# Optimization experiments

Hardware: AMD Instinct MI355X
Metric: run time of the kernel (lower is better)

## Reference

```python
import jax, jax.numpy as jnp
import numpy as np

N = 10000   # nodes
E = 100000  # edges
B = 64      # graphs
HID = 128


def setup_inputs() -> dict:
    key = jax.random.key(0)
    ks = iter(jax.random.split(key, 64))
    def nrm(shape, s=0.1):
        return jax.random.normal(next(ks), shape, dtype=jnp.float32) * s
    inp = {}
    inp["x"] = nrm((N, 1), 1.0)
    inp["node_type"] = jax.random.randint(next(ks), (N,), 0, 2)
    inp["edge_index"] = jax.random.randint(next(ks), (2, E), 0, N)
    inp["edge_attr"] = nrm((E, 1), 1.0)
    inp["batch"] = jnp.sort(jax.random.randint(next(ks), (N,), 0, B))
    inp["vp_w"] = nrm((1, HID)); inp["vp_b"] = nrm((HID,))
    inp["type_emb"] = nrm((2, HID))
    def conv(pre, fin, h, c):
        inp[pre + "_wl"] = nrm((fin, h * c)); inp[pre + "_bl"] = nrm((h * c,))
        inp[pre + "_wr"] = nrm((fin, h * c)); inp[pre + "_br"] = nrm((h * c,))
        inp[pre + "_we"] = nrm((1, h * c));  inp[pre + "_att"] = nrm((h, c))
        inp[pre + "_bias"] = nrm((h * c if pre != "c3" else c,))
    conv("c1", HID, 8, HID)
    conv("c2", HID * 8, 2, HID)
    conv("c3", HID * 2, 1, HID)
    inp["m1_w"] = nrm((HID, HID)); inp["m1_b"] = nrm((HID,))
    inp["ln1_g"] = jnp.ones((HID,), jnp.float32); inp["ln1_b"] = jnp.zeros((HID,), jnp.float32)
    inp["m2_w"] = nrm((HID, HID // 2)); inp["m2_b"] = nrm((HID // 2,))
    inp["ln2_g"] = jnp.ones((HID // 2,), jnp.float32); inp["ln2_b"] = jnp.zeros((HID // 2,), jnp.float32)
    inp["m3_w"] = nrm((HID // 2, 1)); inp["m3_b"] = nrm((1,))
    return inp


def _gatv2(x, src, dst, ea, wl, bl, wr, br, we, att, bias, heads, out_ch, concat):
    """PyG GATv2Conv (eval mode): add self-loops (edge_attr fill='mean' over dst),
    attn = (att * leaky_relu(Wl x_src + Wr x_dst + We e)).sum(-1), segment-softmax
    over destination, scatter-add of alpha * Wl x_src."""
    n = x.shape[0]
    ones = jnp.ones((ea.shape[0], 1), ea.dtype)
    deg = jax.ops.segment_sum(ones, dst, num_segments=n)
    loop_attr = jax.ops.segment_sum(ea, dst, num_segments=n) / jnp.maximum(deg, 1.0)
    ar = jnp.arange(n, dtype=src.dtype)
    src2 = jnp.concatenate([src, ar])
    dst2 = jnp.concatenate([dst, ar])
    ea2 = jnp.concatenate([ea, loop_attr], axis=0)
    xl = (x @ wl + bl).reshape(n, heads, out_ch)   # source transform
    xr = (x @ wr + br).reshape(n, heads, out_ch)   # target transform
    e = (ea2 @ we).reshape(-1, heads, out_ch)      # [E2, H, C]
    msg = xl[src2]                                 # [E2, H, C]
    z = jax.nn.leaky_relu(msg + xr[dst2] + e, 0.2)
    score = jnp.einsum('ehc,hc->eh', z, att)       # [E2, H]
    smax = jax.ops.segment_max(score, dst2, num_segments=n)
    ex = jnp.exp(score - smax[dst2])
    denom = jax.ops.segment_sum(ex, dst2, num_segments=n)
    alpha = ex / denom[dst2]
    out = jax.ops.segment_sum(alpha[:, :, None] * msg, dst2, num_segments=n)
    out = out.reshape(n, heads * out_ch) if concat else out.mean(axis=1)
    return out + bias


def _layernorm(v, g, b):
    mu = v.mean(-1, keepdims=True)
    var = v.var(-1, keepdims=True)
    return (v - mu) / jnp.sqrt(var + 1e-5) * g + b


def reference(x, node_type, edge_index, edge_attr, batch,
              vp_w, vp_b, type_emb,
              c1_wl, c1_bl, c1_wr, c1_br, c1_we, c1_att, c1_bias,
              c2_wl, c2_bl, c2_wr, c2_br, c2_we, c2_att, c2_bias,
              c3_wl, c3_bl, c3_wr, c3_br, c3_we, c3_att, c3_bias,
              m1_w, m1_b, ln1_g, ln1_b, m2_w, m2_b, ln2_g, ln2_b, m3_w, m3_b):
    src, dst = edge_index[0], edge_index[1]
    h = x @ vp_w + vp_b + type_emb[node_type]
    h = jax.nn.leaky_relu(_gatv2(h, src, dst, edge_attr, c1_wl, c1_bl, c1_wr, c1_br, c1_we, c1_att, c1_bias, 8, HID, True), 0.2)
    h = jax.nn.leaky_relu(_gatv2(h, src, dst, edge_attr, c2_wl, c2_bl, c2_wr, c2_br, c2_we, c2_att, c2_bias, 2, HID, True), 0.2)
    h = jax.nn.leaky_relu(_gatv2(h, src, dst, edge_attr, c3_wl, c3_bl, c3_wr, c3_br, c3_we, c3_att, c3_bias, 1, HID, False), 0.2)
    # masked global mean pool over node_type == 0
    w = (node_type == 0).astype(h.dtype)
    sums = jax.ops.segment_sum(h * w[:, None], batch, num_segments=B)
    cnts = jax.ops.segment_sum(w, batch, num_segments=B)
    pooled = sums / jnp.maximum(cnts, 1.0)[:, None]
    h1 = jax.nn.leaky_relu(_layernorm(pooled @ m1_w + m1_b, ln1_g, ln1_b), 0.2)
    h2 = jax.nn.leaky_relu(_layernorm(h1 @ m2_w + m2_b, ln2_g, ln2_b), 0.2)
    return (h2 @ m3_w + m3_b).squeeze(-1)
```

## Files before the change

### kernel.cpp

```cpp
#include <hip/hip_runtime.h>
#include <math.h>

#define NN 10000
#define NE 100000
#define E2 (NE + NN)
#define NBATCH 64

typedef short bf16x8 __attribute__((ext_vector_type(8)));
typedef float f32x4 __attribute__((ext_vector_type(4)));

__device__ __forceinline__ float lrelu(float v){ return fmaxf(v, 0.2f*v); }

__device__ __forceinline__ unsigned short f2bf(float x){
  unsigned int u = __float_as_uint(x);
  u += 0x7fffu + ((u >> 16) & 1u);
  return (unsigned short)(u >> 16);
}
__device__ __forceinline__ float bf2f(unsigned short u){
  return __uint_as_float(((unsigned int)u) << 16);
}

__global__ __launch_bounds__(256) void prep_kernel(
    const float* __restrict__ vp_w, const float* __restrict__ vp_b,
    const float* __restrict__ type_emb,
    const float* __restrict__ c1_wl, const float* __restrict__ c1_bl,
    const float* __restrict__ c1_wr, const float* __restrict__ c1_br,
    float* __restrict__ Ul, float* __restrict__ CTl,
    float* __restrict__ Ur, float* __restrict__ CTr,
    const float* __restrict__ c2_wl, const float* __restrict__ c2_wr,
    const float* __restrict__ c3_wl, const float* __restrict__ c3_wr,
    unsigned short* __restrict__ W2lT, unsigned short* __restrict__ W2rT,
    unsigned short* __restrict__ W3lT, unsigned short* __restrict__ W3rT,
    float* __restrict__ zbase, int zero_words)
{
  __shared__ float t[64][65];
  int b = blockIdx.x;
  int tid = threadIdx.x;
  if (b < 144){
    const float* in; unsigned short* out; int K, N, idx;
    if (b < 64)      { in=c2_wl; out=W2lT; K=1024; N=256; idx=b; }
    else if (b <128) { in=c2_wr; out=W2rT; K=1024; N=256; idx=b-64; }
    else if (b <136) { in=c3_wl; out=W3lT; K=256;  N=128; idx=b-128; }
    else             { in=c3_wr; out=W3rT; K=256;  N=128; idx=b-136; }
    int K64 = K >> 6;
    int kx = idx % K64, nx = idx / K64;
    int k0 = kx*64, n0 = nx*64;
    int lr = tid >> 4;
    int lc = (tid & 15) * 4;
#pragma unroll
    for (int i=0;i<4;++i){
      int r = lr + i*16;
      float4 v = *(const float4*)(in + (size_t)(k0+r)*N + n0 + lc);
      t[r][lc+0]=v.x; t[r][lc+1]=v.y; t[r][lc+2]=v.z; t[r][lc+3]=v.w;
    }
    __syncthreads();
    int sr = tid >> 3;
    int sc = (tid & 7) * 8;
#pragma unroll
    for (int i=0;i<2;++i){
      int n = sr + i*32;
      unsigned short tmp[8];
#pragma unroll
      for (int j=0;j<8;++j) tmp[j] = f2bf(t[sc+j][n]);
      unsigned short* op = out + (size_t)(n0+n)*K + k0 + sc;
      *(ushort4*)op       = make_ushort4(tmp[0],tmp[1],tmp[2],tmp[3]);
      *(ushort4*)(op + 4) = make_ushort4(tmp[4],tmp[5],tmp[6],tmp[7]);
    }
  } else if (b < 148){
    int j = (b-144)*256 + tid;
    float ul=0.f, c0l=0.f, c1l=0.f, ur=0.f, c0r=0.f, c1r=0.f;
    for (int k=0; k<128; ++k){
      float a = c1_wl[k*1024 + j], bb = c1_wr[k*1024 + j];
      float vw = vp_w[k], vb = vp_b[k], t0 = type_emb[k], t1 = type_emb[128+k];
      ul += vw*a; ur += vw*bb;
      c0l += (vb+t0)*a; c1l += (vb+t1)*a;
      c0r += (vb+t0)*bb; c1r += (vb+t1)*bb;
    }
    float bl = c1_bl[j], br = c1_br[j];
    Ul[j]=ul; Ur[j]=ur;
    CTl[j]      = c0l + bl;
    CTl[1024+j] = c1l + bl;
    CTr[j]      = c0r + br;
    CTr[1024+j] = c1r + br;
  } else {
    for (int i = (b-148)*256 + tid; i < zero_words; i += 32*256)
      zbase[i] = 0.f;
  }
}

__global__ void count_kernel(const int* __restrict__ dst, const float* __restrict__ ea,
                             int* __restrict__ deg, float* __restrict__ loop_sum){
  int e = blockIdx.x*256 + threadIdx.x;
  if (e < NE){
    int d = dst[e];
    atomicAdd(&deg[d], 1);
    atomicAdd(&loop_sum[d], ea[e]);
  }
}

__global__ __launch_bounds__(1024) void scan_kernel(const int* __restrict__ deg,
    const float* __restrict__ loop_sum, const float* __restrict__ x,
    const int* __restrict__ ntype,
    int* __restrict__ rowptr, int2* __restrict__ se, float2* __restrict__ xt){
  __shared__ int wtot[16];
  int tid = threadIdx.x;
  int lane = tid & 63, wid = tid >> 6;
  int base = tid*10;
  int d[10]; int run = 0;
#pragma unroll
  for (int j=0;j<10;++j){
    int i = base + j;
    int v = (i < NN) ? deg[i] : 0;
    run += v; d[j] = run;
  }
  int T = run;
  int incl = T;
#pragma unroll
  for (int off=1; off<64; off<<=1){
    int s = __shfl_up(incl, off, 64);
    if (lane >= off) incl += s;
  }
  if (lane == 63) wtot[wid] = incl;
  __syncthreads();
  int wpre = 0;
  for (int w2=0; w2<wid; ++w2) wpre += wtot[w2];
  int ebase = wpre + incl - T;
#pragma unroll
  for (int j=0;j<10;++j){
    int i = base + j;
    if (i < NN){
      int v = d[j] - ((j==0) ? 0 : d[j-1]);
      int rp2 = ebase + d[j] - v + i;
      rowptr[i] = rp2;
      float la = loop_sum[i] / fmaxf((float)v, 1.f);
      se[rp2] = make_int2(i, __float_as_int(la));
      xt[i] = make_float2(x[i], (float)ntype[i]);
    }
  }
  if (tid == 1023){
    int tot = wpre + incl + NN;
    rowptr[NN] = tot;
#pragma unroll
    for (int k=0; k<8; ++k) se[tot+k] = make_int2(0, 0);
  }
}

__global__ void fill_kernel(const int* __restrict__ src, const int* __restrict__ dst,
                            const float* __restrict__ ea, const int* __restrict__ rowptr,
                            int* __restrict__ rowctr, int2* __restrict__ se){
  int e = blockIdx.x*256 + threadIdx.x;
  if (e < NE){
    int d = dst[e];
    int p = rowptr[d] + 1 + atomicAdd(&rowctr[d], 1);
    se[p] = make_int2(src[e], __float_as_int(ea[e]));
  }
}

__global__ __launch_bounds__(256) void conv1_fused(
    const int* __restrict__ rowptr, const int2* __restrict__ se,
    const float2* __restrict__ xt,
    const float* __restrict__ Ul, const float* __restrict__ Ur,
    const float* __restrict__ CTl, const float* __restrict__ CTr,
    const float* __restrict__ we, const float* __restrict__ att,
    const float* __restrict__ bias, unsigned short* __restrict__ out)
{
  int n = blockIdx.x*2 + (threadIdx.x >> 7);
  if (n >= NN) return;
  int te = threadIdx.x & 127;
  int ch0 = te * 8;
  float ul[8], wev[8], a1[8], a2[8], cn0[8], cnd[8];
#pragma unroll
  for (int v=0; v<8; ++v){
    ul[v]=Ul[ch0+v]; wev[v]=we[ch0+v];
    float av = att[ch0+v]; a1[v]=0.6f*av; a2[v]=0.4f*av;
  }
  int beg = rowptr[n], cnt = rowptr[n+1]-beg;
  float2 xtn = xt[n];
  const float* ctr = (xtn.y != 0.f) ? (CTr+1024) : CTr;
#pragma unroll
  for (int v=0; v<8; ++v){
    float c0 = CTl[ch0+v], c1 = CTl[1024+ch0+v];
    cn0[v] = fmaf(xtn.x, Ur[ch0+v], ctr[ch0+v]) + c0;
    cnd[v] = c1 - c0;
  }
  const int2* sp = se + beg;
  int2 q0 = sp[0], q1 = sp[1], q2 = sp[2], q3 = sp[3];
  float2 x0 = xt[q0.x], x1 = xt[q1.x];
  float la_=0.f, lb_=0.f, s1a=0.f, s1b=0.f, sta=0.f, stb=0.f;
  int npair = cnt >> 1;
  for (int p=0; p<npair; ++p){
    int i = p*2;
    float2 x2 = xt[q2.x], x3 = xt[q3.x];
    int2 q4 = sp[i+4], q5 = sp[i+5];
    float xs0=x0.x, tf0=x0.y, ea0=__int_as_float(q0.y);
    float xs1=x1.x, tf1=x1.y, ea1=__int_as_float(q1.y);
    float p0a=0.f,p0b=0.f,p1a=0.f,p1b=0.f;
#pragma unroll
    for (int v=0; v<8; ++v){
      float z0 = fmaf(xs0, ul[v], fmaf(ea0, wev[v], fmaf(tf0, cnd[v], cn0[v])));
      float z1 = fmaf(xs1, ul[v], fmaf(ea1, wev[v], fmaf(tf1, cnd[v], cn0[v])));
      p0a = fmaf(a1[v], z0, p0a); p0b = fmaf(a2[v], fabsf(z0), p0b);
      p1a = fmaf(a1[v], z1, p1a); p1b = fmaf(a2[v], fabsf(z1), p1b);
    }
    float p0 = p0a+p0b, p1 = p1a+p1b;
#pragma unroll
    for (int mm=1; mm<16; mm<<=1){
      p0 += __shfl_xor(p0, mm, 16);
      p1 += __shfl_xor(p1, mm, 16);
    }
    float pe0 = __expf(p0), pe1 = __expf(p1);
    la_ += pe0; lb_ += pe1;
    s1a = fmaf(pe0, xs0, s1a); s1b = fmaf(pe1, xs1, s1b);
    sta = fmaf(pe0, tf0, sta); stb = fmaf(pe1, tf1, stb);
    q0=q2; x0=x2; q1=q3; x1=x3; q2=q4; q3=q5;
  }
  if (cnt & 1){
    float xs0=x0.x, tf0=x0.y, ea0=__int_as_float(q0.y);
    float p0a=0.f,p0b=0.f;
#pragma unroll
    for (int v=0; v<8; ++v){
      float z0 = fmaf(xs0, ul[v], fmaf(ea0, wev[v], fmaf(tf0, cnd[v], cn0[v])));
      p0a = fmaf(a1[v], z0, p0a); p0b = fmaf(a2[v], fabsf(z0), p0b);
    }
    float p0 = p0a+p0b;
#pragma unroll
    for (int mm=1; mm<16; mm<<=1) p0 += __shfl_xor(p0, mm, 16);
    float pe0 = __expf(p0);
    la_ += pe0; s1a = fmaf(pe0, xs0, s1a); sta = fmaf(pe0, tf0, sta);
  }
  float inv = 1.f/(la_+lb_);
  float s1 = (s1a+s1b)*inv;
  float s21 = (sta+stb)*inv;
  float s20 = 1.f - s21;
  bf16x8 ov;
#pragma unroll
  for (int v=0; v<8; ++v){
    float c0 = CTl[ch0+v], c1 = CTl[1024+ch0+v];
    float o = lrelu(fmaf(s1, ul[v], fmaf(s20, c0, fmaf(s21, c1, bias[ch0+v]))));
    ov[v] = (short)f2bf(o);
  }
  *(bf16x8*)(out + (size_t)n*1024 + ch0) = ov;
}

template<int H, int NPB, int VPT, bool ONLY0, bool OUTBF, bool INBF>
__global__ __launch_bounds__(64*NPB) void conv_kernel(
    const int* __restrict__ rowptr, const int2* __restrict__ se,
    const int* __restrict__ ntype,
    const void* __restrict__ Xv, int stride, int xr_off,
    const float* __restrict__ we, const float* __restrict__ att, const float* __restrict__ bias,
    void* __restrict__ out)
{
  const int HC = 64*VPT;
  const int TPH = 64/H;
  int n = blockIdx.x*NPB + (threadIdx.x >> 6);
  if (n >= NN) return;
  if (ONLY0 && ntype[n] != 0) return;
  int tid = threadIdx.x & 63;
  int ch0 = tid * VPT;
  const float* Xf = (const float*)Xv;
  const unsigned short* Xb = (const unsigned short*)Xv;
  float wev[VPT], a1v[VPT], a2v[VPT], biv[VPT], xrv[VPT];
#pragma unroll
  for (int v=0; v<VPT; ++v){
    int ch = ch0+v;
    wev[v]=we[ch]; biv[v]=bias[ch];
    float av = att[ch]; a1v[v]=0.6f*av; a2v[v]=0.4f*av;
  }
  if constexpr (INBF){
    ushort4 q = *(const ushort4*)(Xb + (size_t)n*stride + xr_off + ch0);
    xrv[0]=bf2f(q.x); xrv[1]=bf2f(q.y); xrv[2]=bf2f(q.z); xrv[3]=bf2f(q.w);
  } else {
#pragma unroll
    for (int v=0; v<VPT; ++v) xrv[v]=Xf[(size_t)n*stride + xr_off + ch0+v];
  }
  float ls[4], A[4][VPT];
#pragma unroll
  for (int k=0; k<4; ++k){
    ls[k] = 0.f;
#pragma unroll
    for (int v=0; v<VPT; ++v) A[k][v] = 0.f;
  }
  int beg=rowptr[n], end=rowptr[n+1];
  for (int j=beg; j<end; j+=4){
    bool val[4]; int sx[4]; float ex[4];
#pragma unroll
    for (int k=0; k<4; ++k){
      int pos = j + k;
      val[k] = pos < end;
      int2 q = se[pos];
      sx[k] = q.x; ex[k] = __int_as_float(q.y);
    }
    float xv[4][VPT];
#pragma unroll
    for (int k=0; k<4; ++k){
      if constexpr (INBF){
        ushort4 q = *(const ushort4*)(Xb + (size_t)sx[k]*stride + ch0);
        xv[k][0]=bf2f(q.x); xv[k][1]=bf2f(q.y); xv[k][2]=bf2f(q.z); xv[k][3]=bf2f(q.w);
      } else if constexpr (VPT == 4){
        float4 q = *(const float4*)(Xf + (size_t)sx[k]*stride + ch0);
        xv[k][0]=q.x; xv[k][1]=q.y; xv[k][2]=q.z; xv[k][3]=q.w;
      } else {
        float2 q = *(const float2*)(Xf + (size_t)sx[k]*stride + ch0);
        xv[k][0]=q.x; xv[k][1]=q.y;
      }
    }
    float p[4];
#pragma unroll
    for (int k=0; k<4; ++k){
      float pa = 0.f, pb = 0.f;
#pragma unroll
      for (int v=0; v<VPT; ++v){
        float z = fmaf(ex[k], wev[v], xv[k][v]+xrv[v]);
        pa = fmaf(a1v[v], z, pa);
        pb = fmaf(a2v[v], fabsf(z), pb);
      }
      p[k] = pa + pb;
    }
#pragma unroll
    for (int mm=1; mm<TPH; mm<<=1){
#pragma unroll
      for (int k=0; k<4; ++k) p[k] += __shfl_xor(p[k], mm, 64);
    }
#pragma unroll
    for (int k=0; k<4; ++k){
      float pe = val[k] ? __expf(p[k]) : 0.f;
      ls[k] += pe;
#pragma unroll
      for (int v=0; v<VPT; ++v) A[k][v] = fmaf(pe, xv[k][v], A[k][v]);
    }
  }
  float lt = (ls[0]+ls[1]) + (ls[2]+ls[3]);
  float inv = 1.f/lt;
  size_t baseo=(size_t)n*HC+ch0;
  if constexpr (OUTBF){
    unsigned short* ob = (unsigned short*)out;
    ushort4 o;
    o.x = f2bf(lrelu(((A[0][0]+A[1][0])+(A[2][0]+A[3][0]))*inv+biv[0]));
    o.y = f2bf(lrelu(((A[0][1]+A[1][1])+(A[2][1]+A[3][1]))*inv+biv[1]));
    o.z = f2bf(lrelu(((A[0][2]+A[1][2])+(A[2][2]+A[3][2]))*inv+biv[2]));
    o.w = f2bf(lrelu(((A[0][3]+A[1][3])+(A[2][3]+A[3][3]))*inv+biv[3]));
    *(ushort4*)(ob + baseo) = o;
  } else {
    float* of = (float*)out;
#pragma unroll
    for (int v=0; v<VPT; ++v)
      of[baseo+v] = lrelu(((A[0][v]+A[1][v])+(A[2][v]+A[3][v]))*inv+biv[v]);
  }
}

template<bool OUTBF>
__global__ __launch_bounds__(256) void gemm_dual_lds(
    const short* __restrict__ Abf,
    const short* __restrict__ WlT, const short* __restrict__ WrT,
    const float* __restrict__ bl, const float* __restrict__ br,
    void* __restrict__ Out, int M, int K, int NcH, int cgrid, int rgrid)
{
  __shared__ short lds[12288];
  int id = blockIdx.x;
  int xcd = id & 7, slot = id >> 3;
  int nb = slot % cgrid;
  int rowgroup = (slot / cgrid) * 8 + xcd;
  if (rowgroup >= rgrid) return;
  int row0 = rowgroup * 128;
  int NC2 = 2*NcH;
  int halfx = NcH >> 6;
  int isR = nb >= halfx;
  const short* WT = isR ? WrT : WlT;
  const float* bias = isR ? br : bl;
  int col0 = (nb - (isR ? halfx : 0)) * 64;
  int gcol0 = nb * 64;
  int tid = threadIdx.x;
  int lane = tid & 63, wave = tid >> 6;
  int wm = wave >> 1, wn = wave & 1;
  int quad = lane >> 4, l16 = lane & 15;

  const short* asrc[4];
#pragma unroll
  for (int i=0;i<4;++i){
    int c = wave*256 + i*64 + lane;
    int m = c >> 3, j = c & 7;
    int gr = row0 + m; gr = gr < M ? gr : M-1;
    asrc[i] = Abf + (size_t)gr*K + ((j ^ (m & 7)) << 3);
  }
  const short* bsrc[2];
#pragma unroll
  for (int i=0;i<2;++i){
    int c = wave*128 + i*64 + lane;
    int nloc = c >> 3, j = c & 7;
    bsrc[i] = WT + (size_t)(col0 + nloc)*K + ((j ^ (nloc & 7)) << 3);
  }

  float biasv[2] = { bias[col0 + wn*32 + l16], bias[col0 + wn*32 + 16 + l16] };
  f32x4 acc[4][2];
#pragma unroll
  for (int f=0; f<4; ++f)
#pragma unroll
    for (int g=0; g<2; ++g) acc[f][g] = (f32x4){0.f,0.f,0.f,0.f};

  int niter = K >> 6;
  for (int it=0; it<niter; ++it){
    int k0 = it << 6;
#pragma unroll
    for (int i=0;i<4;++i)
      __builtin_amdgcn_global_load_lds(asrc[i] + k0, &lds[(wave*256 + i*64)*8], 16, 0, 0);
#pragma unroll
    for (int i=0;i<2;++i)
      __builtin_amdgcn_global_load_lds(bsrc[i] + k0, &lds[8192 + (wave*128 + i*64)*8], 16, 0, 0);
    __syncthreads();
#pragma unroll
    for (int s=0; s<2; ++s){
      int t = s*4 + quad;
      bf16x8 af[4], bfv[2];
#pragma unroll
      for (int f=0; f<4; ++f){
        int m = wm*64 + f*16 + l16;
        af[f] = *(const bf16x8*)&lds[m*64 + ((t ^ (m & 7)) << 3)];
      }
#pragma unroll
      for (int g=0; g<2; ++g){
        int nloc = wn*32 + g*16 + l16;
        bfv[g] = *(const bf16x8*)&lds[8192 + nloc*64 + ((t ^ (nloc & 7)) << 3)];
      }
#pragma unroll
      for (int f=0; f<4; ++f)
#pragma unroll
        for (int g=0; g<2; ++g)
          acc[f][g] = __builtin_amdgcn_mfma_f32_16x16x32_bf16(af[f], bfv[g], acc[f][g], 0,0,0);
    }
    __syncthreads();
  }

#pragma unroll
  for (int f=0; f<4; ++f){
    int rbase = row0 + wm*64 + f*16 + quad*4;
#pragma unroll
    for (int r=0; r<4; ++r){
      int rr = rbase + r;
      if (rr < M){
#pragma unroll
        for (int g=0; g<2; ++g){
          int cc = gcol0 + wn*32 + g*16 + l16;
          float val = acc[f][g][r] + biasv[g];
          if constexpr (OUTBF) ((unsigned short*)Out)[(size_t)rr*NC2 + cc] = f2bf(val);
          else                 ((float*)Out)[(size_t)rr*NC2 + cc] = val;
        }
      }
    }
  }
}

__device__ __forceinline__ int lbound(const int* __restrict__ a, int n, int key){
  int lo = 0, hi = n;
  while (lo < hi){ int mid = (lo+hi) >> 1; if (a[mid] < key) lo = mid+1; else hi = mid; }
  return lo;
}

__global__ __launch_bounds__(128) void head_kernel(
    const float* __restrict__ h3, const int* __restrict__ ntype, const int* __restrict__ batch,
    const float* __restrict__ m1w, const float* __restrict__ m1b,
    const float* __restrict__ g1, const float* __restrict__ b1,
    const float* __restrict__ m2w, const float* __restrict__ m2b,
    const float* __restrict__ g2, const float* __restrict__ b2,
    const float* __restrict__ m3w, const float* __restrict__ m3b,
    float* __restrict__ out)
{
  __shared__ float p[128];
  __shared__ float hb[128];
  __shared__ float red[128];
  int b = blockIdx.x, j = threadIdx.x;
  int lo = lbound(batch, NN, b);
  int hi = lbound(batch, NN, b+1);
  float s = 0.f, cnt = 0.f;
  int n = lo;
  for (; n + 3 < hi; n += 4){
    float w0 = (ntype[n]   == 0) ? 1.f : 0.f;
    float w1 = (ntype[n+1] == 0) ? 1.f : 0.f;
    float w2 = (ntype[n+2] == 0) ? 1.f : 0.f;
    float w3 = (ntype[n+3] == 0) ? 1.f : 0.f;
    s += w0*h3[(size_t)n*128 + j]     + w1*h3[(size_t)(n+1)*128 + j]
       + w2*h3[(size_t)(n+2)*128 + j] + w3*h3[(size_t)(n+3)*128 + j];
    cnt += w0 + w1 + w2 + w3;
  }
  for (; n < hi; ++n){
    float w = (ntype[n] == 0) ? 1.f : 0.f;
    s += w*h3[(size_t)n*128 + j];
    cnt += w;
  }
  p[j] = s / fmaxf(cnt, 1.f);
  __syncthreads();
  float a = m1b[j];
  for (int k=0; k<128; ++k) a += p[k]*m1w[k*128 + j];
  red[j] = a; __syncthreads();
  for (int off=64; off>0; off>>=1){ if (j<off) red[j] += red[j+off]; __syncthreads(); }
  float mu = red[0] * (1.f/128.f);
  __syncthreads();
  float d = a - mu;
  red[j] = d*d; __syncthreads();
  for (int off=64; off>0; off>>=1){ if (j<off) red[j] += red[j+off]; __syncthreads(); }
  float var = red[0] * (1.f/128.f);
  __syncthreads();
  hb[j] = lrelu(d * rsqrtf(var + 1e-5f) * g1[j] + b1[j]);
  __syncthreads();
  float a2 = 0.f;
  if (j < 64){
    a2 = m2b[j];
    for (int k=0; k<128; ++k) a2 += hb[k]*m2w[k*64 + j];
  }
  red[j] = (j<64) ? a2 : 0.f; __syncthreads();
  for (int off=64; off>0; off>>=1){ if (j<off) red[j] += red[j+off]; __syncthreads(); }
  float mu2 = red[0] * (1.f/64.f);
  __syncthreads();
  float d2 = a2 - mu2;
  red[j] = (j<64) ? d2*d2 : 0.f; __syncthreads();
  for (int off=64; off>0; off>>=1){ if (j<off) red[j] += red[j+off]; __syncthreads(); }
  float var2 = red[0] * (1.f/64.f);
  __syncthreads();
  if (j < 64) hb[j] = lrelu(d2 * rsqrtf(var2 + 1e-5f) * g2[j] + b2[j]);
  __syncthreads();
  if (j == 0){
    float o = m3b[0];
    for (int k=0; k<64; ++k) o += hb[k]*m3w[k];
    out[b] = o;
  }
}

extern "C" void kernel_launch(void* const* d_in, const int* in_sizes, int n_in,
                              void* d_out, int out_size, void* d_ws, size_t ws_size,
                              hipStream_t stream)
{
  const float* x        = (const float*)d_in[0];
  const int*   ntype    = (const int*)d_in[1];
  const int*   ei       = (const int*)d_in[2];
  const float* eattr    = (const float*)d_in[3];
  const int*   batch    = (const int*)d_in[4];
  const float* vp_w     = (const float*)d_in[5];
  const float* vp_b     = (const float*)d_in[6];
  const float* type_emb = (const float*)d_in[7];
  const float* c1_wl = (const float*)d_in[8];  const float* c1_bl = (const float*)d_in[9];
  const float* c1_wr = (const float*)d_in[10]; const float* c1_br = (const float*)d_in[11];
  const float* c1_we = (const float*)d_in[12]; const float* c1_att= (const float*)d_in[13];
  const float* c1_bias=(const float*)d_in[14];
  const float* c2_wl = (const float*)d_in[15]; const float* c2_bl = (const float*)d_in[16];
  const float* c2_wr = (const float*)d_in[17]; const float* c2_br = (const float*)d_in[18];
  const float* c2_we = (const float*)d_in[19]; const float* c2_att= (const float*)d_in[20];
  const float* c2_bias=(const float*)d_in[21];
  const float* c3_wl = (const float*)d_in[22]; const float* c3_bl = (const float*)d_in[23];
  const float* c3_wr = (const float*)d_in[24]; const float* c3_br = (const float*)d_in[25];
  const float* c3_we = (const float*)d_in[26]; const float* c3_att= (const float*)d_in[27];
  const float* c3_bias=(const float*)d_in[28];
  const float* m1_w = (const float*)d_in[29]; const float* m1_b = (const float*)d_in[30];
  const float* ln1_g= (const float*)d_in[31]; const float* ln1_b= (const float*)d_in[32];
  const float* m2_w = (const float*)d_in[33]; const float* m2_b = (const float*)d_in[34];
  const float* ln2_g= (const float*)d_in[35]; const float* ln2_b= (const float*)d_in[36];
  const float* m3_w = (const float*)d_in[37]; const float* m3_b = (const float*)d_in[38];
  const int* esrc = ei;
  const int* edst = ei + NE;
  float* outp = (float*)d_out;
  (void)in_sizes; (void)n_in; (void)out_size; (void)ws_size;

  char* w = (char*)d_ws;
  auto alloc = [&](size_t bytes) -> void* {
    void* p = (void*)w;
    w += (bytes + 255) & ~(size_t)255;
    return p;
  };
  unsigned short* h1bf = (unsigned short*)alloc((size_t)NN*1024*2);
  unsigned short* X2   = (unsigned short*)alloc((size_t)NN*512*2);
  unsigned short* h2bf = (unsigned short*)alloc((size_t)NN*256*2);
  float* X3   = (float*)alloc((size_t)NN*256*4);
  float* h3   = (float*)alloc((size_t)NN*128*4);
  unsigned short* W2lT = (unsigned short*)alloc((size_t)256*1024*2);
  unsigned short* W2rT = (unsigned short*)alloc((size_t)256*1024*2);
  unsigned short* W3lT = (unsigned short*)alloc((size_t)128*256*2);
  unsigned short* W3rT = (unsigned short*)alloc((size_t)128*256*2);
  float* Ul   = (float*)alloc(1024*4);
  float* CTl  = (float*)alloc(2048*4);
  float* Ur   = (float*)alloc(1024*4);
  float* CTr  = (float*)alloc(2048*4);
  const int zero_words = 3*NN;
  float* zbase = (float*)alloc((size_t)zero_words*4);
  int*   deg      = (int*)zbase;
  int*   rowctr   = (int*)(zbase + NN);
  float* loop_sum = zbase + 2*NN;
  float2* xt      = (float2*)alloc((size_t)NN*8);
  int*   rowptr   = (int*)alloc((size_t)(NN+1)*4);
  int2*  se       = (int2*)alloc((size_t)(E2+8)*8);

  prep_kernel<<<180, 256, 0, stream>>>(vp_w, vp_b, type_emb,
      c1_wl, c1_bl, c1_wr, c1_br, Ul, CTl, Ur, CTr,
      c2_wl, c2_wr, c3_wl, c3_wr, W2lT, W2rT, W3lT, W3rT,
      zbase, zero_words);
  count_kernel<<<(NE+255)/256, 256, 0, stream>>>(edst, eattr, deg, loop_sum);
  scan_kernel<<<1, 1024, 0, stream>>>(deg, loop_sum, x, ntype, rowptr, se, xt);
  fill_kernel<<<(NE+255)/256, 256, 0, stream>>>(esrc, edst, eattr, rowptr, rowctr, se);
  conv1_fused<<<NN/2, 256, 0, stream>>>(rowptr, se, xt,
      Ul, Ur, CTl, CTr, c1_we, c1_att, c1_bias, h1bf);
  gemm_dual_lds<true><<<640, 256, 0, stream>>>(
      (const short*)h1bf, (const short*)W2lT, (const short*)W2rT, c2_bl, c2_br,
      (void*)X2, NN, 1024, 256, 8, 79);
  conv_kernel<2,4,4,false,true,true><<<NN/4, 256, 0, stream>>>(rowptr, se, ntype,
      (const void*)X2, 512, 256, c2_we, c2_att, c2_bias, h2bf);
  gemm_dual_lds<false><<<320, 256, 0, stream>>>(
      (const short*)h2bf, (const short*)W3lT, (const short*)W3rT, c3_bl, c3_br,
      (void*)X3, NN, 256, 128, 4, 79);
  conv_kernel<1,4,2,true,false,false><<<NN/4, 256, 0, stream>>>(rowptr, se, ntype,
      (const void*)X3, 256, 128, c3_we, c3_att, c3_bias, h3);
  head_kernel<<<NBATCH, 128, 0, stream>>>(h3, ntype, batch, m1_w, m1_b, ln1_g, ln1_b,
                                          m2_w, m2_b, ln2_g, ln2_b, m3_w, m3_b, outp);
}
```

Measured before the change: 311.0 us.

## Stage node features in LDS and make conv1 a persistent grid-stride kernel

conv1_fused now copies the whole per-node (x, type) float2 table, 80KB, into shared memory once per block. All neighbour gathers then read LDS instead of global memory. The kernel becomes persistent: a fixed grid of 512 blocks walks over node pairs, so per-channel constants stay in registers and are loaded once per block instead of once per node. In exchange, every block pays the 80KB copy, and the large LDS footprint limits occupancy to about one block per CU. The branchy CTr select is also replaced by an FMA.

```diff
diff --git a/kernel.cpp b/kernel.cpp
--- a/kernel.cpp
+++ b/kernel.cpp
@@ -164,82 +164,93 @@
     const float* __restrict__ we, const float* __restrict__ att,
     const float* __restrict__ bias, unsigned short* __restrict__ out)
 {
-  int n = blockIdx.x*2 + (threadIdx.x >> 7);
-  if (n >= NN) return;
-  int te = threadIdx.x & 127;
+  __shared__ float2 sxt[NN];
+  int tid = threadIdx.x;
+  for (int i = tid; i < NN/2; i += 256)
+    ((float4*)sxt)[i] = ((const float4*)xt)[i];
+  __syncthreads();
+  int te = tid & 127;
+  int half = tid >> 7;
   int ch0 = te * 8;
-  float ul[8], wev[8], a1[8], a2[8], cn0[8], cnd[8];
+  float ul[8], wev[8], a1[8], a2[8], ctl0[8], ctl1[8], ctr0[8], ctrd[8], urv[8];
 #pragma unroll
   for (int v=0; v<8; ++v){
     ul[v]=Ul[ch0+v]; wev[v]=we[ch0+v];
     float av = att[ch0+v]; a1[v]=0.6f*av; a2[v]=0.4f*av;
-  }
-  int beg = rowptr[n], cnt = rowptr[n+1]-beg;
-  float2 xtn = xt[n];
-  const float* ctr = (xtn.y != 0.f) ? (CTr+1024) : CTr;
-#pragma unroll
-  for (int v=0; v<8; ++v){
-    float c0 = CTl[ch0+v], c1 = CTl[1024+ch0+v];
-    cn0[v] = fmaf(xtn.x, Ur[ch0+v], ctr[ch0+v]) + c0;
-    cnd[v] = c1 - c0;
-  }
-  const int2* sp = se + beg;
-  int2 q0 = sp[0], q1 = sp[1], q2 = sp[2], q3 = sp[3];
-  float2 x0 = xt[q0.x], x1 = xt[q1.x];
-  float la_=0.f, lb_=0.f, s1a=0.f, s1b=0.f, sta=0.f, stb=0.f;
-  int npair = cnt >> 1;
-  for (int p=0; p<npair; ++p){
-    int i = p*2;
-    float2 x2 = xt[q2.x], x3 = xt[q3.x];
-    int2 q4 = sp[i+4], q5 = sp[i+5];
-    float xs0=x0.x, tf0=x0.y, ea0=__int_as_float(q0.y);
-    float xs1=x1.x, tf1=x1.y, ea1=__int_as_float(q1.y);
-    float p0a=0.f,p0b=0.f,p1a=0.f,p1b=0.f;
+    ctl0[v]=CTl[ch0+v]; ctl1[v]=CTl[1024+ch0+v];
+    float r0 = CTr[ch0+v], r1 = CTr[1024+ch0+v];
+    ctr0[v]=r0; ctrd[v]=r1-r0;
+    urv[v]=Ur[ch0+v];
+  }
+  const int stride = gridDim.x*2;
+  for (int n0 = blockIdx.x*2; n0 < NN; n0 += stride){
+    int n = n0 + half;
+    int beg = rowptr[n], cnt = rowptr[n+1]-beg;
+    float2 xtn = sxt[n];
+    float cn0[8], cnd[8];
 #pragma unroll
     for (int v=0; v<8; ++v){
-      float z0 = fmaf(xs0, ul[v], fmaf(ea0, wev[v], fmaf(tf0, cnd[v], cn0[v])));
-      float z1 = fmaf(xs1, ul[v], fmaf(ea1, wev[v], fmaf(tf1, cnd[v], cn0[v])));
-      p0a = fmaf(a1[v], z0, p0a); p0b = fmaf(a2[v], fabsf(z0), p0b);
-      p1a = fmaf(a1[v], z1, p1a); p1b = fmaf(a2[v], fabsf(z1), p1b);
-    }
-    float p0 = p0a+p0b, p1 = p1a+p1b;
-#pragma unroll
-    for (int mm=1; mm<16; mm<<=1){
-      p0 += __shfl_xor(p0, mm, 16);
-      p1 += __shfl_xor(p1, mm, 16);
-    }
-    float pe0 = __expf(p0), pe1 = __expf(p1);
-    la_ += pe0; lb_ += pe1;
-    s1a = fmaf(pe0, xs0, s1a); s1b = fmaf(pe1, xs1, s1b);
-    sta = fmaf(pe0, tf0, sta); stb = fmaf(pe1, tf1, stb);
-    q0=q2; x0=x2; q1=q3; x1=x3; q2=q4; q3=q5;
-  }
-  if (cnt & 1){
-    float xs0=x0.x, tf0=x0.y, ea0=__int_as_float(q0.y);
-    float p0a=0.f,p0b=0.f;
+      float ctr = fmaf(xtn.y, ctrd[v], ctr0[v]);
+      cn0[v] = fmaf(xtn.x, urv[v], ctr) + ctl0[v];
+      cnd[v] = ctl1[v] - ctl0[v];
+    }
+    const int2* sp = se + beg;
+    int2 q0 = sp[0], q1 = sp[1], q2 = sp[2], q3 = sp[3];
+    float2 x0 = sxt[q0.x], x1 = sxt[q1.x];
+    float la_=0.f, lb_=0.f, s1a=0.f, s1b=0.f, sta=0.f, stb=0.f;
+    int npair = cnt >> 1;
+    for (int p=0; p<npair; ++p){
+      int i = p*2;
+      float2 x2 = sxt[q2.x], x3 = sxt[q3.x];
+      int2 q4 = sp[i+4], q5 = sp[i+5];
+      float xs0=x0.x, tf0=x0.y, ea0=__int_as_float(q0.y);
+      float xs1=x1.x, tf1=x1.y, ea1=__int_as_float(q1.y);
+      float p0a=0.f,p0b=0.f,p1a=0.f,p1b=0.f;
+#pragma unroll
+      for (int v=0; v<8; ++v){
+        float z0 = fmaf(xs0, ul[v], fmaf(ea0, wev[v], fmaf(tf0, cnd[v], cn0[v])));
+        float z1 = fmaf(xs1, ul[v], fmaf(ea1, wev[v], fmaf(tf1, cnd[v], cn0[v])));
+        p0a = fmaf(a1[v], z0, p0a); p0b = fmaf(a2[v], fabsf(z0), p0b);
+        p1a = fmaf(a1[v], z1, p1a); p1b = fmaf(a2[v], fabsf(z1), p1b);
+      }
+      float p0 = p0a+p0b, p1 = p1a+p1b;
+#pragma unroll
+      for (int mm=1; mm<16; mm<<=1){
+        p0 += __shfl_xor(p0, mm, 16);
+        p1 += __shfl_xor(p1, mm, 16);
+      }
+      float pe0 = __expf(p0), pe1 = __expf(p1);
+      la_ += pe0; lb_ += pe1;
+      s1a = fmaf(pe0, xs0, s1a); s1b = fmaf(pe1, xs1, s1b);
+      sta = fmaf(pe0, tf0, sta); stb = fmaf(pe1, tf1, stb);
+      q0=q2; x0=x2; q1=q3; x1=x3; q2=q4; q3=q5;
+    }
+    if (cnt & 1){
+      float xs0=x0.x, tf0=x0.y, ea0=__int_as_float(q0.y);
+      float p0a=0.f,p0b=0.f;
+#pragma unroll
+      for (int v=0; v<8; ++v){
+        float z0 = fmaf(xs0, ul[v], fmaf(ea0, wev[v], fmaf(tf0, cnd[v], cn0[v])));
+        p0a = fmaf(a1[v], z0, p0a); p0b = fmaf(a2[v], fabsf(z0), p0b);
+      }
+      float p0 = p0a+p0b;
+#pragma unroll
+      for (int mm=1; mm<16; mm<<=1) p0 += __shfl_xor(p0, mm, 16);
+      float pe0 = __expf(p0);
+      la_ += pe0; s1a = fmaf(pe0, xs0, s1a); sta = fmaf(pe0, tf0, sta);
+    }
+    float inv = 1.f/(la_+lb_);
+    float s1 = (s1a+s1b)*inv;
+    float s21 = (sta+stb)*inv;
+    float s20 = 1.f - s21;
+    bf16x8 ov;
 #pragma unroll
     for (int v=0; v<8; ++v){
-      float z0 = fmaf(xs0, ul[v], fmaf(ea0, wev[v], fmaf(tf0, cnd[v], cn0[v])));
-      p0a = fmaf(a1[v], z0, p0a); p0b = fmaf(a2[v], fabsf(z0), p0b);
-    }
-    float p0 = p0a+p0b;
-#pragma unroll
-    for (int mm=1; mm<16; mm<<=1) p0 += __shfl_xor(p0, mm, 16);
-    float pe0 = __expf(p0);
-    la_ += pe0; s1a = fmaf(pe0, xs0, s1a); sta = fmaf(pe0, tf0, sta);
-  }
-  float inv = 1.f/(la_+lb_);
-  float s1 = (s1a+s1b)*inv;
-  float s21 = (sta+stb)*inv;
-  float s20 = 1.f - s21;
-  bf16x8 ov;
-#pragma unroll
-  for (int v=0; v<8; ++v){
-    float c0 = CTl[ch0+v], c1 = CTl[1024+ch0+v];
-    float o = lrelu(fmaf(s1, ul[v], fmaf(s20, c0, fmaf(s21, c1, bias[ch0+v]))));
-    ov[v] = (short)f2bf(o);
-  }
-  *(bf16x8*)(out + (size_t)n*1024 + ch0) = ov;
+      float o = lrelu(fmaf(s1, ul[v], fmaf(s20, ctl0[v], fmaf(s21, ctl1[v], bias[ch0+v]))));
+      ov[v] = (short)f2bf(o);
+    }
+    *(bf16x8*)(out + (size_t)n*1024 + ch0) = ov;
+  }
 }
 
 template<int H, int NPB, int VPT, bool ONLY0, bool OUTBF, bool INBF>
@@ -593,7 +604,7 @@
   count_kernel<<<(NE+255)/256, 256, 0, stream>>>(edst, eattr, deg, loop_sum);
   scan_kernel<<<1, 1024, 0, stream>>>(deg, loop_sum, x, ntype, rowptr, se, xt);
   fill_kernel<<<(NE+255)/256, 256, 0, stream>>>(esrc, edst, eattr, rowptr, rowctr, se);
-  conv1_fused<<<NN/2, 256, 0, stream>>>(rowptr, se, xt,
+  conv1_fused<<<512, 256, 0, stream>>>(rowptr, se, xt,
       Ul, Ur, CTl, CTr, c1_we, c1_att, c1_bias, h1bf);
   gemm_dual_lds<true><<<640, 256, 0, stream>>>(
       (const short*)h1bf, (const short*)W2lT, (const short*)W2rT, c2_bl, c2_br,
```

New measurement: 322.7 us. 3.8% more time.
